# Optimization experiments

Hardware: AMD Instinct MI355X
Metric: run time of the kernel (lower is better)

Reference implementation:

```python
import jax, jax.numpy as jnp
import numpy as np

BINS = jnp.array([1, 2, 3, 4, 8, 16, 32, 64], dtype=jnp.int32)
L = 10      # max span width
HID = 150   # Score hidden dim


def _mlp(x, W1, b1, W2, b2, W3, b3):
    # Score module: Linear -> ReLU -> Linear -> ReLU -> Linear (dropout = identity at eval)
    h = jax.nn.relu(x @ W1 + b1)
    h = jax.nn.relu(h @ W2 + b2)
    return h @ W3 + b3


def setup_inputs() -> dict:
    key = jax.random.key(0)
    ks = jax.random.split(key, 16)
    T, A, E, D, S = 8192, 1024, 512, 20, 32768
    GI = 2 * A + E + D  # 2580
    sc = lambda n: 1.0 / np.sqrt(n)
    return {
        "states": jax.random.normal(ks[0], (T, A), jnp.float32),
        "embeds": jax.random.normal(ks[1], (T, E), jnp.float32),
        "span_starts": jnp.sort(jax.random.randint(ks[2], (S,), 0, T - L)),
        "span_lengths": jax.random.randint(ks[3], (S,), 0, L),
        # attention Score params (attn_dim -> 150 -> 150 -> 1)
        "Wa1": jax.random.normal(ks[4], (A, HID), jnp.float32) * sc(A),
        "ba1": jnp.zeros((HID,), jnp.float32),
        "Wa2": jax.random.normal(ks[5], (HID, HID), jnp.float32) * sc(HID),
        "ba2": jnp.zeros((HID,), jnp.float32),
        "Wa3": jax.random.normal(ks[6], (HID, 1), jnp.float32) * sc(HID),
        "ba3": jnp.zeros((1,), jnp.float32),
        # Distance embedding table (len(bins)+1 = 9 buckets)
        "width_table": jax.random.normal(ks[7], (9, D), jnp.float32) * 0.1,
        # mention Score params (gi_dim -> 150 -> 150 -> 1)
        "Ws1": jax.random.normal(ks[8], (GI, HID), jnp.float32) * sc(GI),
        "bs1": jnp.zeros((HID,), jnp.float32),
        "Ws2": jax.random.normal(ks[9], (HID, HID), jnp.float32) * sc(HID),
        "bs2": jnp.zeros((HID,), jnp.float32),
        "Ws3": jax.random.normal(ks[10], (HID, 1), jnp.float32) * sc(HID),
        "bs3": jnp.zeros((1,), jnp.float32),
    }


def reference(states, embeds, span_starts, span_lengths,
              Wa1, ba1, Wa2, ba2, Wa3, ba3,
              width_table,
              Ws1, bs1, Ws2, bs2, Ws3, bs3):
    T = states.shape[0]
    # per-token attention logits: [T, 1]
    attns = _mlp(states, Wa1, ba1, Wa2, ba2, Wa3, ba3)

    pos = jnp.arange(L)
    idx = span_starts[:, None] + pos[None, :]                 # [S, L]
    mask = pos[None, :] <= span_lengths[:, None]              # valid positions
    idx = jnp.minimum(idx, T - 1)

    span_attn = jnp.where(mask, attns[idx, 0], -jnp.inf)      # [S, L]
    w = jax.nn.softmax(span_attn, axis=1)                     # per-span softmax
    pooled = jnp.einsum('sl,sle->se', w, embeds[idx])         # [S, E]

    ends = span_starts + span_lengths
    widths = span_lengths + 1
    bucket = jnp.searchsorted(BINS, widths.astype(jnp.int32), side='right')
    size_emb = width_table[bucket]                            # [S, D]

    g = jnp.concatenate([states[span_starts], states[ends], pooled, size_emb], axis=-1)
    scores = _mlp(g, Ws1, bs1, Ws2, bs2, Ws3, bs3)[:, 0]      # [S]
    return scores
```

## Files before the change

kernel.cpp:

```cpp
#include <hip/hip_runtime.h>
#include <math.h>

#define T_TOK 8192
#define A_DIM 1024
#define E_DIM 512
#define S_SPAN 32768
#define HID 150

typedef __attribute__((ext_vector_type(8))) short short8;
typedef __attribute__((ext_vector_type(4))) float f32x4;
typedef __attribute__((ext_vector_type(4))) unsigned int u32x4;
typedef __attribute__((ext_vector_type(4))) unsigned short u16x4;

__device__ __forceinline__ unsigned short f2bf(float f) {
    unsigned int u = __builtin_bit_cast(unsigned int, f);
    u += 0x7FFFu + ((u >> 16) & 1u);
    return (unsigned short)(u >> 16);
}
__device__ __forceinline__ float bf2f(unsigned int h16) {
    unsigned int u = h16 << 16;
    return __builtin_bit_cast(float, u);
}

#define NS4 (T_TOK * A_DIM / 4)
#define NE4 (T_TOK * E_DIM / 4)
#define NCAST ((NS4 + NE4) / 256)

struct WConv { const float* src; unsigned short* dst; int K0; int Kpad; int nblk; };
struct PrepTab {
    const float* s; const float* e; unsigned short* sd; unsigned short* ed;
    WConv g[6];
    const float* wt; const float* Ws1w; float* PW;
};

__global__ __launch_bounds__(256) void prep_kernel(PrepTab tab) {
    __shared__ unsigned short tile[64 * 161];
    int b = blockIdx.x;
    if (b < NCAST) {
        int idx = b * 256 + threadIdx.x;
        const float* src; unsigned short* dst;
        if (idx < NS4) { src = tab.s; dst = tab.sd; }
        else { idx -= NS4; src = tab.e; dst = tab.ed; }
        f32x4 v = *(const f32x4*)(src + (size_t)idx * 4);
        u16x4 o;
        o.x = f2bf(v.x); o.y = f2bf(v.y); o.z = f2bf(v.z); o.w = f2bf(v.w);
        *(u16x4*)(dst + (size_t)idx * 4) = o;
        return;
    }
    b -= NCAST;
    #pragma unroll
    for (int gi = 0; gi < 6; ++gi) {
        if (b < tab.g[gi].nblk) {
            const int k0 = b * 64;
            const int K0 = tab.g[gi].K0, Kpad = tab.g[gi].Kpad;
            const float* src = tab.g[gi].src;
            unsigned short* dst = tab.g[gi].dst;
            for (int idx = threadIdx.x; idx < 64 * 160; idx += 256) {
                int kr = idx / 160, j = idx - kr * 160;
                int k = k0 + kr;
                float v = (j < HID && k < K0) ? src[(size_t)k * HID + j] : 0.f;
                tile[kr * 161 + j] = f2bf(v);
            }
            __syncthreads();
            for (int idx = threadIdx.x; idx < 160 * 64; idx += 256) {
                int j = idx >> 6, kc = idx & 63;
                dst[(size_t)j * Kpad + k0 + kc] = tile[kc * 161 + j];
            }
            return;
        }
        b -= tab.g[gi].nblk;
    }
    int j = threadIdx.x;
    if (j < HID) {
        float acc = 0.f;
        for (int k = 0; k < 20; ++k)
            acc = fmaf(tab.wt[b * 20 + k], tab.Ws1w[k * HID + j], acc);
        tab.PW[b * HID + j] = acc;
    }
}

struct GG {
    const unsigned short* A; int lda;
    const unsigned short* W; int K; int nrb;
    unsigned short* outh; int ldo;
    const float* bias; int relu;
    const float* dotv; const float* dotb; float* dotout;
};
struct GTab { GG g[4]; int ng; };

__global__ __launch_bounds__(256) void gemm_fused(GTab tab) {
    constexpr int LDW = 88;
    __shared__ unsigned short WtL[2][160 * LDW];

    int b = blockIdx.x;
    int gi = 0;
    while (gi < tab.ng - 1 && b >= tab.g[gi].nrb) { b -= tab.g[gi].nrb; ++gi; }
    const GG G = tab.g[gi];

    const int tid = threadIdx.x;
    const int wid = tid >> 6;
    const int lane = tid & 63;
    const int l15 = lane & 15;
    const int quad = lane >> 4;
    const int row0 = b * 64 + wid * 16 + l15;
    const int K = G.K;
    const int nch = K >> 6;
    const unsigned short* Arow = G.A + (size_t)row0 * G.lda;

    u32x4 stg[5];
    int sn[5], sk[5];
    #pragma unroll
    for (int i = 0; i < 5; ++i) { int u = tid + i * 256; sn[i] = u >> 3; sk[i] = (u & 7) * 8; }

    f32x4 acc[10];
    #pragma unroll
    for (int nt = 0; nt < 10; ++nt) acc[nt] = (f32x4){0.f, 0.f, 0.f, 0.f};

    #pragma unroll
    for (int i = 0; i < 5; ++i)
        stg[i] = *(const u32x4*)(G.W + (size_t)sn[i] * K + sk[i]);
    short8 avc0 = *(const short8*)(Arow + quad * 8);
    short8 avc1 = *(const short8*)(Arow + 32 + quad * 8);
    #pragma unroll
    for (int i = 0; i < 5; ++i)
        *(u32x4*)&WtL[0][sn[i] * LDW + sk[i]] = stg[i];
    __syncthreads();

    for (int c = 0; c < nch; ++c) {
        const int pb = c & 1;
        short8 avn0, avn1;
        const bool more = (c + 1 < nch);
        if (more) {
            const int kn = (c + 1) << 6;
            #pragma unroll
            for (int i = 0; i < 5; ++i)
                stg[i] = *(const u32x4*)(G.W + (size_t)sn[i] * K + kn + sk[i]);
            avn0 = *(const short8*)(Arow + kn + quad * 8);
            avn1 = *(const short8*)(Arow + kn + 32 + quad * 8);
        }
        #pragma unroll
        for (int nt = 0; nt < 10; ++nt) {
            short8 bv0 = *(const short8*)&WtL[pb][(nt * 16 + l15) * LDW + quad * 8];
            acc[nt] = __builtin_amdgcn_mfma_f32_16x16x32_bf16(avc0, bv0, acc[nt], 0, 0, 0);
            short8 bv1 = *(const short8*)&WtL[pb][(nt * 16 + l15) * LDW + 32 + quad * 8];
            acc[nt] = __builtin_amdgcn_mfma_f32_16x16x32_bf16(avc1, bv1, acc[nt], 0, 0, 0);
        }
        if (more) {
            #pragma unroll
            for (int i = 0; i < 5; ++i)
                *(u32x4*)&WtL[pb ^ 1][sn[i] * LDW + sk[i]] = stg[i];
            avc0 = avn0; avc1 = avn1;
        }
        __syncthreads();
    }

    const int rbase = b * 64 + wid * 16 + quad * 4;
    if (G.dotout) {
        float part[4] = {0.f, 0.f, 0.f, 0.f};
        #pragma unroll
        for (int nt = 0; nt < 10; ++nt) {
            int col = nt * 16 + l15;
            float bv_ = (col < HID) ? G.bias[col] : 0.f;
            float vv = (col < HID) ? G.dotv[col] : 0.f;
            #pragma unroll
            for (int r = 0; r < 4; ++r)
                part[r] += fmaxf(acc[nt][r] + bv_, 0.f) * vv;
        }
        #pragma unroll
        for (int r = 0; r < 4; ++r) {
            float p = part[r];
            #pragma unroll
            for (int off = 1; off < 16; off <<= 1) p += __shfl_xor(p, off);
            if (l15 == 0) G.dotout[rbase + r] = p + G.dotb[0];
        }
    } else {
        #pragma unroll
        for (int nt = 0; nt < 10; ++nt) {
            int col = nt * 16 + l15;
            float bv_ = (G.bias != nullptr && col < HID) ? G.bias[col] : 0.f;
            #pragma unroll
            for (int r = 0; r < 4; ++r) {
                int row = rbase + r;
                float v = acc[nt][r] + bv_;
                if (G.relu) v = fmaxf(v, 0.f);
                G.outh[(size_t)row * G.ldo + col] = f2bf(v);
            }
        }
    }
}

__global__ __launch_bounds__(256) void span_l1_kernel(const float* __restrict__ attns,
                                                      const int* __restrict__ starts,
                                                      const int* __restrict__ lens,
                                                      const unsigned short* __restrict__ Ps,
                                                      const unsigned short* __restrict__ Pe,
                                                      const unsigned short* __restrict__ Pm,
                                                      const float* __restrict__ PW,
                                                      const float* __restrict__ bs1,
                                                      unsigned short* __restrict__ SH1) {
    const int wid = threadIdx.x >> 6, lane = threadIdx.x & 63;
    const int s = blockIdx.x * 4 + wid;
    const int start = starts[s];
    const int len = lens[s];

    const int iv = min(start + lane, T_TOK - 1);
    float a = (lane <= len) ? attns[iv] : -INFINITY;
    float m = a;
    #pragma unroll
    for (int off = 32; off; off >>= 1) m = fmaxf(m, __shfl_xor(m, off));
    float e = (lane <= len) ? __expf(a - m) : 0.f;
    float ssum = e;
    #pragma unroll
    for (int off = 32; off; off >>= 1) ssum += __shfl_xor(ssum, off);
    float wv = e / ssum;

    float wl[10]; int il[10];
    #pragma unroll
    for (int l = 0; l < 10; ++l) { wl[l] = __shfl(wv, l); il[l] = __shfl(iv, l); }

    const int end = start + len;
    const int width = len + 1;
    const int bucket = (width >= 1) + (width >= 2) + (width >= 3) + (width >= 4) +
                       (width >= 8) + (width >= 16) + (width >= 32) + (width >= 64);

    const unsigned short* ps = Ps + (size_t)start * 160;
    const unsigned short* pe = Pe + (size_t)end * 160;
    const float* pw = PW + bucket * HID;

    for (int p = lane; p < 75; p += 64) {
        const int j = 2 * p;
        unsigned int u0 = *(const unsigned int*)(ps + j);
        unsigned int u1 = *(const unsigned int*)(pe + j);
        float a0 = bs1[j]     + bf2f(u0 & 0xffff) + bf2f(u1 & 0xffff) + pw[j];
        float a1 = bs1[j + 1] + bf2f(u0 >> 16)    + bf2f(u1 >> 16)    + pw[j + 1];
        #pragma unroll
        for (int l = 0; l < 10; ++l) {
            unsigned int um = *(const unsigned int*)(Pm + (size_t)il[l] * 160 + j);
            a0 = fmaf(wl[l], bf2f(um & 0xffff), a0);
            a1 = fmaf(wl[l], bf2f(um >> 16), a1);
        }
        unsigned int packed = (unsigned int)f2bf(fmaxf(a0, 0.f)) |
                              ((unsigned int)f2bf(fmaxf(a1, 0.f)) << 16);
        *(unsigned int*)(SH1 + (size_t)s * 192 + j) = packed;
    }
}

extern "C" void kernel_launch(void* const* d_in, const int* in_sizes, int n_in,
                              void* d_out, int out_size, void* d_ws, size_t ws_size,
                              hipStream_t stream) {
    const float* states = (const float*)d_in[0];
    const float* embeds = (const float*)d_in[1];
    const int* span_starts = (const int*)d_in[2];
    const int* span_lengths = (const int*)d_in[3];
    const float* Wa1 = (const float*)d_in[4];
    const float* ba1 = (const float*)d_in[5];
    const float* Wa2 = (const float*)d_in[6];
    const float* ba2 = (const float*)d_in[7];
    const float* Wa3 = (const float*)d_in[8];
    const float* ba3 = (const float*)d_in[9];
    const float* width_table = (const float*)d_in[10];
    const float* Ws1 = (const float*)d_in[11];
    const float* bs1 = (const float*)d_in[12];
    const float* Ws2 = (const float*)d_in[13];
    const float* bs2 = (const float*)d_in[14];
    const float* Ws3 = (const float*)d_in[15];
    const float* bs3 = (const float*)d_in[16];
    float* out = (float*)d_out;

    char* w = (char*)d_ws;
    unsigned short* WtA  = (unsigned short*)w;  w += 480 * 1024 * 2;
    unsigned short* WtE  = (unsigned short*)w;  w += 160 * 512 * 2;
    unsigned short* Wa2t = (unsigned short*)w;  w += 160 * 192 * 2;
    unsigned short* Ws2t = (unsigned short*)w;  w += 160 * 192 * 2;
    float* PW    = (float*)w;                   w += 5632;
    float* attns = (float*)w;                   w += 8192 * 4;
    unsigned short* Sbf = (unsigned short*)w;   w += (size_t)T_TOK * A_DIM * 2;
    unsigned short* Ebf = (unsigned short*)w;   w += (size_t)T_TOK * E_DIM * 2;
    unsigned short* Psh = (unsigned short*)w;   w += (size_t)T_TOK * 160 * 2;
    unsigned short* Peh = (unsigned short*)w;   w += (size_t)T_TOK * 160 * 2;
    unsigned short* Pmh = (unsigned short*)w;   w += (size_t)T_TOK * 160 * 2;
    unsigned short* H1A = (unsigned short*)w;   w += (size_t)T_TOK * 192 * 2;
    unsigned short* SH1 = (unsigned short*)w;   w += (size_t)S_SPAN * 192 * 2;

    PrepTab pt;
    pt.s = states; pt.e = embeds; pt.sd = Sbf; pt.ed = Ebf;
    pt.g[0] = { Wa1,              WtA,              1024, 1024, 16 };
    pt.g[1] = { Ws1,              WtA + 160*1024,   1024, 1024, 16 };
    pt.g[2] = { Ws1 + 1024*150,   WtA + 320*1024,   1024, 1024, 16 };
    pt.g[3] = { Ws1 + 2048*150,   WtE,               512,  512,  8 };
    pt.g[4] = { Wa2,              Wa2t,              150,  192,  3 };
    pt.g[5] = { Ws2,              Ws2t,              150,  192,  3 };
    pt.wt = width_table; pt.Ws1w = Ws1 + 2560*150; pt.PW = PW;
    prep_kernel<<<NCAST + 62 + 9, 256, 0, stream>>>(pt);

    GG z = {};

    GTab t1; t1.ng = 4;
    t1.g[0] = z; t1.g[0].A = Sbf; t1.g[0].lda = 1024; t1.g[0].W = WtA;            t1.g[0].K = 1024;
    t1.g[0].nrb = 128; t1.g[0].outh = H1A; t1.g[0].ldo = 192; t1.g[0].bias = ba1; t1.g[0].relu = 1;
    t1.g[1] = z; t1.g[1].A = Sbf; t1.g[1].lda = 1024; t1.g[1].W = WtA + 160*1024; t1.g[1].K = 1024;
    t1.g[1].nrb = 128; t1.g[1].outh = Psh; t1.g[1].ldo = 160;
    t1.g[2] = z; t1.g[2].A = Sbf; t1.g[2].lda = 1024; t1.g[2].W = WtA + 320*1024; t1.g[2].K = 1024;
    t1.g[2].nrb = 128; t1.g[2].outh = Peh; t1.g[2].ldo = 160;
    t1.g[3] = z; t1.g[3].A = Ebf; t1.g[3].lda = 512;  t1.g[3].W = WtE;            t1.g[3].K = 512;
    t1.g[3].nrb = 128; t1.g[3].outh = Pmh; t1.g[3].ldo = 160;
    gemm_fused<<<512, 256, 0, stream>>>(t1);

    GTab t2; t2.ng = 1;
    t2.g[0] = z; t2.g[0].A = H1A; t2.g[0].lda = 192; t2.g[0].W = Wa2t; t2.g[0].K = 192;
    t2.g[0].nrb = 128; t2.g[0].bias = ba2; t2.g[0].dotv = Wa3; t2.g[0].dotb = ba3; t2.g[0].dotout = attns;
    gemm_fused<<<128, 256, 0, stream>>>(t2);

    span_l1_kernel<<<S_SPAN / 4, 256, 0, stream>>>(attns, span_starts, span_lengths,
                                                   Psh, Peh, Pmh, PW, bs1, SH1);

    GTab t3; t3.ng = 1;
    t3.g[0] = z; t3.g[0].A = SH1; t3.g[0].lda = 192; t3.g[0].W = Ws2t; t3.g[0].K = 192;
    t3.g[0].nrb = 512; t3.g[0].bias = bs2; t3.g[0].dotv = Ws3; t3.g[0].dotb = bs3; t3.g[0].dotout = out;
    gemm_fused<<<512, 256, 0, stream>>>(t3);
}
```

Before: 191.1 us.

## Fuse fp32-to-bf16 activation cast into GEMM A-loads and shrink K chunk

Drops the separate pass that cast states and embeds to bf16 in the prep kernel. The GEMM now reads fp32 activations directly and converts them to bf16 in registers while loading the A operand. K chunks shrink from 64 to 32, with a smaller LDS tile and a launch-bounds occupancy hint. This removes a full write and re-read of the bf16 activation copies, but the GEMM now reads twice the bytes per A element and repeats the conversion for each of the four column groups that share the states input.

```diff
diff --git a/kernel.cpp b/kernel.cpp
--- a/kernel.cpp
+++ b/kernel.cpp
@@ -10,7 +10,6 @@
 typedef __attribute__((ext_vector_type(8))) short short8;
 typedef __attribute__((ext_vector_type(4))) float f32x4;
 typedef __attribute__((ext_vector_type(4))) unsigned int u32x4;
-typedef __attribute__((ext_vector_type(4))) unsigned short u16x4;
 
 __device__ __forceinline__ unsigned short f2bf(float f) {
     unsigned int u = __builtin_bit_cast(unsigned int, f);
@@ -22,13 +21,8 @@
     return __builtin_bit_cast(float, u);
 }
 
-#define NS4 (T_TOK * A_DIM / 4)
-#define NE4 (T_TOK * E_DIM / 4)
-#define NCAST ((NS4 + NE4) / 256)
-
 struct WConv { const float* src; unsigned short* dst; int K0; int Kpad; int nblk; };
 struct PrepTab {
-    const float* s; const float* e; unsigned short* sd; unsigned short* ed;
     WConv g[6];
     const float* wt; const float* Ws1w; float* PW;
 };
@@ -36,18 +30,6 @@
 __global__ __launch_bounds__(256) void prep_kernel(PrepTab tab) {
     __shared__ unsigned short tile[64 * 161];
     int b = blockIdx.x;
-    if (b < NCAST) {
-        int idx = b * 256 + threadIdx.x;
-        const float* src; unsigned short* dst;
-        if (idx < NS4) { src = tab.s; dst = tab.sd; }
-        else { idx -= NS4; src = tab.e; dst = tab.ed; }
-        f32x4 v = *(const f32x4*)(src + (size_t)idx * 4);
-        u16x4 o;
-        o.x = f2bf(v.x); o.y = f2bf(v.y); o.z = f2bf(v.z); o.w = f2bf(v.w);
-        *(u16x4*)(dst + (size_t)idx * 4) = o;
-        return;
-    }
-    b -= NCAST;
     #pragma unroll
     for (int gi = 0; gi < 6; ++gi) {
         if (b < tab.g[gi].nblk) {
@@ -80,7 +62,7 @@
 }
 
 struct GG {
-    const unsigned short* A; int lda;
+    const void* A; int lda; int a_fp32;
     const unsigned short* W; int K; int nrb;
     unsigned short* outh; int ldo;
     const float* bias; int relu;
@@ -88,8 +70,25 @@
 };
 struct GTab { GG g[4]; int ng; };
 
-__global__ __launch_bounds__(256) void gemm_fused(GTab tab) {
-    constexpr int LDW = 88;
+__device__ __forceinline__ short8 loadA(const void* A, int a_fp32, size_t row, int lda, int kk) {
+    short8 r;
+    if (a_fp32) {
+        const float* p = (const float*)A + row * (size_t)lda + kk;
+        f32x4 f0 = *(const f32x4*)p;
+        f32x4 f1 = *(const f32x4*)(p + 4);
+        r[0] = (short)f2bf(f0.x); r[1] = (short)f2bf(f0.y);
+        r[2] = (short)f2bf(f0.z); r[3] = (short)f2bf(f0.w);
+        r[4] = (short)f2bf(f1.x); r[5] = (short)f2bf(f1.y);
+        r[6] = (short)f2bf(f1.z); r[7] = (short)f2bf(f1.w);
+    } else {
+        const unsigned short* p = (const unsigned short*)A + row * (size_t)lda + kk;
+        r = *(const short8*)p;
+    }
+    return r;
+}
+
+__global__ __launch_bounds__(256, 4) void gemm_fused(GTab tab) {
+    constexpr int LDW = 40;
     __shared__ unsigned short WtL[2][160 * LDW];
 
     int b = blockIdx.x;
@@ -102,54 +101,53 @@
     const int lane = tid & 63;
     const int l15 = lane & 15;
     const int quad = lane >> 4;
-    const int row0 = b * 64 + wid * 16 + l15;
+    const size_t row0 = b * 64 + wid * 16 + l15;
     const int K = G.K;
-    const int nch = K >> 6;
-    const unsigned short* Arow = G.A + (size_t)row0 * G.lda;
-
-    u32x4 stg[5];
-    int sn[5], sk[5];
-    #pragma unroll
-    for (int i = 0; i < 5; ++i) { int u = tid + i * 256; sn[i] = u >> 3; sk[i] = (u & 7) * 8; }
+    const int nch = K >> 5;
+
+    u32x4 stg[3];
+    int sn[3], sk[3];
+    #pragma unroll
+    for (int i = 0; i < 3; ++i) { int u = tid + i * 256; sn[i] = u >> 2; sk[i] = (u & 3) * 8; }
 
     f32x4 acc[10];
     #pragma unroll
     for (int nt = 0; nt < 10; ++nt) acc[nt] = (f32x4){0.f, 0.f, 0.f, 0.f};
 
     #pragma unroll
-    for (int i = 0; i < 5; ++i)
-        stg[i] = *(const u32x4*)(G.W + (size_t)sn[i] * K + sk[i]);
-    short8 avc0 = *(const short8*)(Arow + quad * 8);
-    short8 avc1 = *(const short8*)(Arow + 32 + quad * 8);
-    #pragma unroll
-    for (int i = 0; i < 5; ++i)
-        *(u32x4*)&WtL[0][sn[i] * LDW + sk[i]] = stg[i];
+    for (int i = 0; i < 3; ++i)
+        if (tid + i * 256 < 640)
+            stg[i] = *(const u32x4*)(G.W + (size_t)sn[i] * K + sk[i]);
+    short8 avc = loadA(G.A, G.a_fp32, row0, G.lda, quad * 8);
+    #pragma unroll
+    for (int i = 0; i < 3; ++i)
+        if (tid + i * 256 < 640)
+            *(u32x4*)&WtL[0][sn[i] * LDW + sk[i]] = stg[i];
     __syncthreads();
 
     for (int c = 0; c < nch; ++c) {
         const int pb = c & 1;
-        short8 avn0, avn1;
+        short8 avn;
         const bool more = (c + 1 < nch);
         if (more) {
-            const int kn = (c + 1) << 6;
-            #pragma unroll
-            for (int i = 0; i < 5; ++i)
-                stg[i] = *(const u32x4*)(G.W + (size_t)sn[i] * K + kn + sk[i]);
-            avn0 = *(const short8*)(Arow + kn + quad * 8);
-            avn1 = *(const short8*)(Arow + kn + 32 + quad * 8);
+            const int kn = (c + 1) << 5;
+            #pragma unroll
+            for (int i = 0; i < 3; ++i)
+                if (tid + i * 256 < 640)
+                    stg[i] = *(const u32x4*)(G.W + (size_t)sn[i] * K + kn + sk[i]);
+            avn = loadA(G.A, G.a_fp32, row0, G.lda, kn + quad * 8);
         }
         #pragma unroll
         for (int nt = 0; nt < 10; ++nt) {
-            short8 bv0 = *(const short8*)&WtL[pb][(nt * 16 + l15) * LDW + quad * 8];
-            acc[nt] = __builtin_amdgcn_mfma_f32_16x16x32_bf16(avc0, bv0, acc[nt], 0, 0, 0);
-            short8 bv1 = *(const short8*)&WtL[pb][(nt * 16 + l15) * LDW + 32 + quad * 8];
-            acc[nt] = __builtin_amdgcn_mfma_f32_16x16x32_bf16(avc1, bv1, acc[nt], 0, 0, 0);
+            short8 bv = *(const short8*)&WtL[pb][(nt * 16 + l15) * LDW + quad * 8];
+            acc[nt] = __builtin_amdgcn_mfma_f32_16x16x32_bf16(avc, bv, acc[nt], 0, 0, 0);
         }
         if (more) {
             #pragma unroll
-            for (int i = 0; i < 5; ++i)
-                *(u32x4*)&WtL[pb ^ 1][sn[i] * LDW + sk[i]] = stg[i];
-            avc0 = avn0; avc1 = avn1;
+            for (int i = 0; i < 3; ++i)
+                if (tid + i * 256 < 640)
+                    *(u32x4*)&WtL[pb ^ 1][sn[i] * LDW + sk[i]] = stg[i];
+            avc = avn;
         }
         __syncthreads();
     }
@@ -274,8 +272,6 @@
     unsigned short* Ws2t = (unsigned short*)w;  w += 160 * 192 * 2;
     float* PW    = (float*)w;                   w += 5632;
     float* attns = (float*)w;                   w += 8192 * 4;
-    unsigned short* Sbf = (unsigned short*)w;   w += (size_t)T_TOK * A_DIM * 2;
-    unsigned short* Ebf = (unsigned short*)w;   w += (size_t)T_TOK * E_DIM * 2;
     unsigned short* Psh = (unsigned short*)w;   w += (size_t)T_TOK * 160 * 2;
     unsigned short* Peh = (unsigned short*)w;   w += (size_t)T_TOK * 160 * 2;
     unsigned short* Pmh = (unsigned short*)w;   w += (size_t)T_TOK * 160 * 2;
@@ -283,7 +279,6 @@
     unsigned short* SH1 = (unsigned short*)w;   w += (size_t)S_SPAN * 192 * 2;
 
     PrepTab pt;
-    pt.s = states; pt.e = embeds; pt.sd = Sbf; pt.ed = Ebf;
     pt.g[0] = { Wa1,              WtA,              1024, 1024, 16 };
     pt.g[1] = { Ws1,              WtA + 160*1024,   1024, 1024, 16 };
     pt.g[2] = { Ws1 + 1024*150,   WtA + 320*1024,   1024, 1024, 16 };
@@ -291,31 +286,37 @@
     pt.g[4] = { Wa2,              Wa2t,              150,  192,  3 };
     pt.g[5] = { Ws2,              Ws2t,              150,  192,  3 };
     pt.wt = width_table; pt.Ws1w = Ws1 + 2560*150; pt.PW = PW;
-    prep_kernel<<<NCAST + 62 + 9, 256, 0, stream>>>(pt);
+    prep_kernel<<<62 + 9, 256, 0, stream>>>(pt);
 
     GG z = {};
 
     GTab t1; t1.ng = 4;
-    t1.g[0] = z; t1.g[0].A = Sbf; t1.g[0].lda = 1024; t1.g[0].W = WtA;            t1.g[0].K = 1024;
-    t1.g[0].nrb = 128; t1.g[0].outh = H1A; t1.g[0].ldo = 192; t1.g[0].bias = ba1; t1.g[0].relu = 1;
-    t1.g[1] = z; t1.g[1].A = Sbf; t1.g[1].lda = 1024; t1.g[1].W = WtA + 160*1024; t1.g[1].K = 1024;
-    t1.g[1].nrb = 128; t1.g[1].outh = Psh; t1.g[1].ldo = 160;
-    t1.g[2] = z; t1.g[2].A = Sbf; t1.g[2].lda = 1024; t1.g[2].W = WtA + 320*1024; t1.g[2].K = 1024;
-    t1.g[2].nrb = 128; t1.g[2].outh = Peh; t1.g[2].ldo = 160;
-    t1.g[3] = z; t1.g[3].A = Ebf; t1.g[3].lda = 512;  t1.g[3].W = WtE;            t1.g[3].K = 512;
-    t1.g[3].nrb = 128; t1.g[3].outh = Pmh; t1.g[3].ldo = 160;
+    t1.g[0] = z; t1.g[0].A = states; t1.g[0].lda = 1024; t1.g[0].a_fp32 = 1;
+    t1.g[0].W = WtA;            t1.g[0].K = 1024; t1.g[0].nrb = 128;
+    t1.g[0].outh = H1A; t1.g[0].ldo = 192; t1.g[0].bias = ba1; t1.g[0].relu = 1;
+    t1.g[1] = z; t1.g[1].A = states; t1.g[1].lda = 1024; t1.g[1].a_fp32 = 1;
+    t1.g[1].W = WtA + 160*1024; t1.g[1].K = 1024; t1.g[1].nrb = 128;
+    t1.g[1].outh = Psh; t1.g[1].ldo = 160;
+    t1.g[2] = z; t1.g[2].A = states; t1.g[2].lda = 1024; t1.g[2].a_fp32 = 1;
+    t1.g[2].W = WtA + 320*1024; t1.g[2].K = 1024; t1.g[2].nrb = 128;
+    t1.g[2].outh = Peh; t1.g[2].ldo = 160;
+    t1.g[3] = z; t1.g[3].A = embeds; t1.g[3].lda = 512;  t1.g[3].a_fp32 = 1;
+    t1.g[3].W = WtE;            t1.g[3].K = 512;  t1.g[3].nrb = 128;
+    t1.g[3].outh = Pmh; t1.g[3].ldo = 160;
     gemm_fused<<<512, 256, 0, stream>>>(t1);
 
     GTab t2; t2.ng = 1;
-    t2.g[0] = z; t2.g[0].A = H1A; t2.g[0].lda = 192; t2.g[0].W = Wa2t; t2.g[0].K = 192;
-    t2.g[0].nrb = 128; t2.g[0].bias = ba2; t2.g[0].dotv = Wa3; t2.g[0].dotb = ba3; t2.g[0].dotout = attns;
+    t2.g[0] = z; t2.g[0].A = H1A; t2.g[0].lda = 192; t2.g[0].a_fp32 = 0;
+    t2.g[0].W = Wa2t; t2.g[0].K = 192; t2.g[0].nrb = 128;
+    t2.g[0].bias = ba2; t2.g[0].dotv = Wa3; t2.g[0].dotb = ba3; t2.g[0].dotout = attns;
     gemm_fused<<<128, 256, 0, stream>>>(t2);
 
     span_l1_kernel<<<S_SPAN / 4, 256, 0, stream>>>(attns, span_starts, span_lengths,
                                                    Psh, Peh, Pmh, PW, bs1, SH1);
 
     GTab t3; t3.ng = 1;
-    t3.g[0] = z; t3.g[0].A = SH1; t3.g[0].lda = 192; t3.g[0].W = Ws2t; t3.g[0].K = 192;
-    t3.g[0].nrb = 512; t3.g[0].bias = bs2; t3.g[0].dotv = Ws3; t3.g[0].dotb = bs3; t3.g[0].dotout = out;
+    t3.g[0] = z; t3.g[0].A = SH1; t3.g[0].lda = 192; t3.g[0].a_fp32 = 0;
+    t3.g[0].W = Ws2t; t3.g[0].K = 192; t3.g[0].nrb = 512;
+    t3.g[0].bias = bs2; t3.g[0].dotv = Ws3; t3.g[0].dotb = bs3; t3.g[0].dotout = out;
     gemm_fused<<<512, 256, 0, stream>>>(t3);
 }
```

Result: slower. 206.3 us (+7.9%).
